# Performance work log

Measured on AMD Instinct MI355X. Metric: run time of the kernel, lower is better.

## Reference

```python
import jax, jax.numpy as jnp
import numpy as np


def _compute_features(ff):
    # ff: (..., 4) = [rx, ry, rvx, rvy]
    rx, ry, rvx, rvy = ff[..., 0], ff[..., 1], ff[..., 2], ff[..., 3]
    dist_sq = rx * rx + ry * ry
    dist = jnp.sqrt(dist_sq + 1e-06)
    inv_dist = 1.0 / (dist + 0.1)
    dir_x = rx / (dist + 1e-06)
    dir_y = ry / (dist + 1e-06)
    speed_sq = rvx * rvx + rvy * rvy
    rel_speed = jnp.sqrt(speed_sq + 1e-06)
    dot_vp = rvx * rx + rvy * ry
    closing_speed = dot_vp / (dist + 1e-06)
    ttca = jnp.tanh(-dot_vp / (speed_sq + 1e-06))
    return jnp.stack(
        [rx, ry, rvx, rvy, dist, inv_dist, rel_speed, closing_speed,
         dir_x, dir_y, ttca, dot_vp], axis=-1)  # (..., 12)


def setup_inputs() -> dict:
    key = jax.random.key(0)
    k0, k1, k2, k3, k4 = jax.random.split(key, 5)
    B, N, H, HID, IN = 16, 256, 8, 64, 12
    ff = jax.random.normal(k0, (B, N, N, 4), dtype=jnp.float32)
    # nn.Linear default init scale ~ 1/sqrt(fan_in); use small random weights
    W1 = jax.random.normal(k1, (IN, HID), dtype=jnp.float32) / np.sqrt(IN)
    b1 = jax.random.normal(k2, (HID,), dtype=jnp.float32) / np.sqrt(IN)
    W2 = jax.random.normal(k3, (HID, H), dtype=jnp.float32) / np.sqrt(HID)
    b2 = jax.random.normal(k4, (H,), dtype=jnp.float32) / np.sqrt(HID)
    return {"fundamental_features": ff, "W1": W1, "b1": b1, "W2": W2, "b2": b2}


def reference(fundamental_features, W1, b1, W2, b2):
    feats = _compute_features(fundamental_features)          # (B, N, N, 12)
    h = jax.nn.silu(jnp.einsum('bnmf,fh->bnmh', feats, W1) + b1)  # (B, N, N, 64)
    bias = jnp.einsum('bnmh,ho->bnmo', h, W2) + b2            # (B, N, N, H)
    return jnp.transpose(bias, (0, 3, 1, 2))                  # (B, H, N, N)
```

## Files before the change

kernel.cpp:

```cpp
#include <hip/hip_runtime.h>

#define NH 8
#define HID 64
#define NPAIRS (16 * 256 * 256)
#define BLOCK 256
#define GPW 4
#define LSTR 68

typedef __attribute__((ext_vector_type(8))) short bf16x8;
typedef __attribute__((ext_vector_type(4))) float f32x4;
typedef __attribute__((ext_vector_type(16))) float f32x16;

union F8 { bf16x8 v; unsigned u[4]; uint4 q4; };

__device__ __host__ inline unsigned bfpk(float a, float b) {
    unsigned ua = __float_as_uint(a); ua += 0x7fffu + ((ua >> 16) & 1u);
    unsigned ub = __float_as_uint(b); ub += 0x7fffu + ((ub >> 16) & 1u);
    return (ua >> 16) | (ub & 0xffff0000u);
}

__global__ void pack_weights(const float* __restrict__ W1, const float* __restrict__ b1,
                             const float* __restrict__ W2, const float* __restrict__ b2,
                             unsigned char* __restrict__ ws) {
    int l = threadIdx.x;
    int n32 = l & 31, q2 = l >> 5;
    int n16 = l & 15, q4 = l >> 4;
    unsigned* B1 = (unsigned*)ws;
    unsigned* B2 = (unsigned*)(ws + 2048);
    float* b1v = (float*)(ws + 4096);
    float* b2v = (float*)(ws + 4608);
    for (int m = 0; m < 2; ++m) {
        int h = m * 32 + n32;
        for (int j2 = 0; j2 < 4; ++j2) {
            int k0 = q2 * 8 + 2 * j2;
            float v0 = (k0 < 12) ? W1[k0 * HID + h] : 0.f;
            float v1 = (k0 + 1 < 12) ? W1[(k0 + 1) * HID + h] : 0.f;
            B1[(m * 64 + l) * 4 + j2] = bfpk(v0, v1);
        }
        b1v[m * 64 + l] = b1[h];
    }
    for (int kc = 0; kc < 2; ++kc)
        for (int j2 = 0; j2 < 4; ++j2) {
            int k0 = kc * 32 + q4 * 8 + 2 * j2;
            float v0 = (n16 < NH) ? W2[k0 * NH + n16] : 0.f;
            float v1 = (n16 < NH) ? W2[(k0 + 1) * NH + n16] : 0.f;
            B2[(kc * 64 + l) * 4 + j2] = bfpk(v0, v1);
        }
    b2v[l] = (n16 < NH) ? b2[n16] : 0.f;
}

__global__ __launch_bounds__(BLOCK) void relfeat_mfma2(
    const float* __restrict__ ff, const unsigned char* __restrict__ ws,
    float* __restrict__ out)
{
    __shared__ float lds[4][32 * LSTR];
    const int tid = threadIdx.x;
    const int w = tid >> 6, l = tid & 63;
    const int n32 = l & 31, q2 = l >> 5;
    const int n16 = l & 15, q4 = l >> 4;
    float* my = lds[w];

    F8 B1f[2], B2f[2];
    #pragma unroll
    for (int m = 0; m < 2; ++m)  B1f[m].q4 = ((const uint4*)ws)[m * 64 + l];
    #pragma unroll
    for (int kc = 0; kc < 2; ++kc) B2f[kc].q4 = ((const uint4*)(ws + 2048))[kc * 64 + l];
    float b1s[2];
    b1s[0] = ((const float*)(ws + 4096))[l];
    b1s[1] = ((const float*)(ws + 4096))[64 + l];
    const float b2s = ((const float*)(ws + 4608))[l];

    f32x16 cbias[2];
    #pragma unroll
    for (int m = 0; m < 2; ++m)
        #pragma unroll
        for (int r = 0; r < 16; ++r) cbias[m][r] = b1s[m];

    const int wave_base = (blockIdx.x * 4 + w) * (GPW * 32);

    for (int g = 0; g < GPW; ++g) {
        const int pbase = wave_base + g * 32;

        float4 v = ((const float4*)ff)[pbase + n32];
        float rx = v.x, ry = v.y, rvx = v.z, rvy = v.w;
        float dist_sq = rx * rx + ry * ry;
        float dist = sqrtf(dist_sq + 1e-6f);
        float speed_sq = rvx * rvx + rvy * rvy;
        float dot_vp = rvx * rx + rvy * ry;
        float invd = __builtin_amdgcn_rcpf(dist + 1e-6f);
        float inv_dist = __builtin_amdgcn_rcpf(dist + 0.1f);
        float rel_speed = sqrtf(speed_sq + 1e-6f);
        float closing = dot_vp * invd;
        float dir_x = rx * invd, dir_y = ry * invd;
        float z = -dot_vp * __builtin_amdgcn_rcpf(speed_sq + 1e-6f);
        float ez = __expf(2.f * z);
        float ttca = 1.f - 2.f * __builtin_amdgcn_rcpf(ez + 1.f);

        F8 a1;
        a1.u[0] = (q2 == 0) ? bfpk(rx, ry)          : bfpk(dir_x, dir_y);
        a1.u[1] = (q2 == 0) ? bfpk(rvx, rvy)        : bfpk(ttca, dot_vp);
        a1.u[2] = (q2 == 0) ? bfpk(dist, inv_dist)  : 0u;
        a1.u[3] = (q2 == 0) ? bfpk(rel_speed, closing) : 0u;

        #pragma unroll
        for (int m = 0; m < 2; ++m) {
            f32x16 d1 = __builtin_amdgcn_mfma_f32_32x32x16_bf16(a1.v, B1f[m].v, cbias[m], 0, 0, 0);
            #pragma unroll
            for (int r = 0; r < 16; ++r) {
                int prow = (r & 3) + 8 * (r >> 2) + 4 * q2;
                float x = d1[r];
                float s = x * __builtin_amdgcn_rcpf(1.f + __expf(-x));
                my[prow * LSTR + m * 32 + n32] = s;
            }
        }

        #pragma unroll
        for (int hl = 0; hl < 2; ++hl) {
            f32x4 d2 = {b2s, b2s, b2s, b2s};
            #pragma unroll
            for (int kc = 0; kc < 2; ++kc) {
                const float* rp = &my[(hl * 16 + n16) * LSTR + kc * 32 + q4 * 8];
                float4 lo = *(const float4*)rp;
                float4 hi = *(const float4*)(rp + 4);
                F8 a2;
                a2.u[0] = bfpk(lo.x, lo.y); a2.u[1] = bfpk(lo.z, lo.w);
                a2.u[2] = bfpk(hi.x, hi.y); a2.u[3] = bfpk(hi.z, hi.w);
                d2 = __builtin_amdgcn_mfma_f32_16x16x32_bf16(a2.v, B2f[kc].v, d2, 0, 0, 0);
            }
            if (n16 < NH) {
                int p0 = pbase + hl * 16 + q4 * 4;
                int b = p0 >> 16, lo16 = p0 & 65535;
                float4 st; st.x = d2[0]; st.y = d2[1]; st.z = d2[2]; st.w = d2[3];
                *(float4*)(out + (size_t)b * (NH * 65536) + (size_t)n16 * 65536 + lo16) = st;
            }
        }
    }
}

extern "C" void kernel_launch(void* const* d_in, const int* in_sizes, int n_in,
                              void* d_out, int out_size, void* d_ws, size_t ws_size,
                              hipStream_t stream) {
    const float* ff = (const float*)d_in[0];
    const float* W1 = (const float*)d_in[1];
    const float* b1 = (const float*)d_in[2];
    const float* W2 = (const float*)d_in[3];
    const float* b2 = (const float*)d_in[4];
    float* out = (float*)d_out;
    unsigned char* ws = (unsigned char*)d_ws;

    pack_weights<<<1, 64, 0, stream>>>(W1, b1, W2, b2, ws);
    const int grid = NPAIRS / (32 * GPW * 4);
    relfeat_mfma2<<<grid, BLOCK, 0, stream>>>(ff, ws, out);
}
```

Measured before the change: 104.8 us.

## Compute features once per lane, fold b1 into GEMM, store hidden as bf16 in LDS

```diff
diff --git a/kernel.cpp b/kernel.cpp
--- a/kernel.cpp
+++ b/kernel.cpp
@@ -1,11 +1,11 @@
 #include <hip/hip_runtime.h>
+#include <hip/hip_bf16.h>
 
 #define NH 8
 #define HID 64
 #define NPAIRS (16 * 256 * 256)
 #define BLOCK 256
-#define GPW 4
-#define LSTR 68
+#define LROW 72
 
 typedef __attribute__((ext_vector_type(8))) short bf16x8;
 typedef __attribute__((ext_vector_type(4))) float f32x4;
@@ -13,10 +13,11 @@
 
 union F8 { bf16x8 v; unsigned u[4]; uint4 q4; };
 
-__device__ __host__ inline unsigned bfpk(float a, float b) {
-    unsigned ua = __float_as_uint(a); ua += 0x7fffu + ((ua >> 16) & 1u);
-    unsigned ub = __float_as_uint(b); ub += 0x7fffu + ((ub >> 16) & 1u);
-    return (ua >> 16) | (ub & 0xffff0000u);
+__device__ inline unsigned pk2(float a, float b) {
+    __hip_bfloat162 h = __float22bfloat162_rn(make_float2(a, b));
+    unsigned u;
+    __builtin_memcpy(&u, &h, 4);
+    return u;
 }
 
 __global__ void pack_weights(const float* __restrict__ W1, const float* __restrict__ b1,
@@ -27,64 +28,57 @@
     int n16 = l & 15, q4 = l >> 4;
     unsigned* B1 = (unsigned*)ws;
     unsigned* B2 = (unsigned*)(ws + 2048);
-    float* b1v = (float*)(ws + 4096);
-    float* b2v = (float*)(ws + 4608);
+    float* b2v = (float*)(ws + 4096);
     for (int m = 0; m < 2; ++m) {
         int h = m * 32 + n32;
         for (int j2 = 0; j2 < 4; ++j2) {
-            int k0 = q2 * 8 + 2 * j2;
-            float v0 = (k0 < 12) ? W1[k0 * HID + h] : 0.f;
-            float v1 = (k0 + 1 < 12) ? W1[(k0 + 1) * HID + h] : 0.f;
-            B1[(m * 64 + l) * 4 + j2] = bfpk(v0, v1);
+            int k0 = q2 * 8 + 2 * j2, k1 = k0 + 1;
+            float v0 = (k0 < 12) ? W1[k0 * HID + h] : (k0 == 12 ? b1[h] : 0.f);
+            float v1 = (k1 < 12) ? W1[k1 * HID + h] : 0.f;
+            B1[(m * 64 + l) * 4 + j2] = pk2(v0, v1);
         }
-        b1v[m * 64 + l] = b1[h];
     }
     for (int kc = 0; kc < 2; ++kc)
         for (int j2 = 0; j2 < 4; ++j2) {
             int k0 = kc * 32 + q4 * 8 + 2 * j2;
             float v0 = (n16 < NH) ? W2[k0 * NH + n16] : 0.f;
             float v1 = (n16 < NH) ? W2[(k0 + 1) * NH + n16] : 0.f;
-            B2[(kc * 64 + l) * 4 + j2] = bfpk(v0, v1);
+            B2[(kc * 64 + l) * 4 + j2] = pk2(v0, v1);
         }
     b2v[l] = (n16 < NH) ? b2[n16] : 0.f;
 }
 
-__global__ __launch_bounds__(BLOCK) void relfeat_mfma2(
+__global__ __launch_bounds__(BLOCK) void relfeat_mfma3(
     const float* __restrict__ ff, const unsigned char* __restrict__ ws,
     float* __restrict__ out)
 {
-    __shared__ float lds[4][32 * LSTR];
+    __shared__ unsigned short lds[4][32 * LROW];
     const int tid = threadIdx.x;
     const int w = tid >> 6, l = tid & 63;
     const int n32 = l & 31, q2 = l >> 5;
     const int n16 = l & 15, q4 = l >> 4;
-    float* my = lds[w];
+    unsigned short* my = lds[w];
 
     F8 B1f[2], B2f[2];
+    B1f[0].q4 = ((const uint4*)ws)[l];
+    B1f[1].q4 = ((const uint4*)ws)[64 + l];
+    B2f[0].q4 = ((const uint4*)(ws + 2048))[l];
+    B2f[1].q4 = ((const uint4*)(ws + 2048))[64 + l];
+    const float b2s = ((const float*)(ws + 4096))[l];
+
+    f32x16 z16;
     #pragma unroll
-    for (int m = 0; m < 2; ++m)  B1f[m].q4 = ((const uint4*)ws)[m * 64 + l];
+    for (int r = 0; r < 16; ++r) z16[r] = 0.f;
+
+    const int wave_base = (blockIdx.x * 4 + w) * 128;
+
     #pragma unroll
-    for (int kc = 0; kc < 2; ++kc) B2f[kc].q4 = ((const uint4*)(ws + 2048))[kc * 64 + l];
-    float b1s[2];
-    b1s[0] = ((const float*)(ws + 4096))[l];
-    b1s[1] = ((const float*)(ws + 4096))[64 + l];
-    const float b2s = ((const float*)(ws + 4608))[l];
+    for (int it = 0; it < 2; ++it) {
+        const int pbase = wave_base + it * 64;
 
-    f32x16 cbias[2];
-    #pragma unroll
-    for (int m = 0; m < 2; ++m)
-        #pragma unroll
-        for (int r = 0; r < 16; ++r) cbias[m][r] = b1s[m];
-
-    const int wave_base = (blockIdx.x * 4 + w) * (GPW * 32);
-
-    for (int g = 0; g < GPW; ++g) {
-        const int pbase = wave_base + g * 32;
-
-        float4 v = ((const float4*)ff)[pbase + n32];
+        float4 v = ((const float4*)ff)[pbase + l];
         float rx = v.x, ry = v.y, rvx = v.z, rvy = v.w;
-        float dist_sq = rx * rx + ry * ry;
-        float dist = sqrtf(dist_sq + 1e-6f);
+        float dist = sqrtf(rx * rx + ry * ry + 1e-6f);
         float speed_sq = rvx * rvx + rvy * rvy;
         float dot_vp = rvx * rx + rvy * ry;
         float invd = __builtin_amdgcn_rcpf(dist + 1e-6f);
@@ -92,46 +86,63 @@
         float rel_speed = sqrtf(speed_sq + 1e-6f);
         float closing = dot_vp * invd;
         float dir_x = rx * invd, dir_y = ry * invd;
-        float z = -dot_vp * __builtin_amdgcn_rcpf(speed_sq + 1e-6f);
-        float ez = __expf(2.f * z);
+        float zz = -dot_vp * __builtin_amdgcn_rcpf(speed_sq + 1e-6f);
+        float ez = __expf(2.f * zz);
         float ttca = 1.f - 2.f * __builtin_amdgcn_rcpf(ez + 1.f);
 
-        F8 a1;
-        a1.u[0] = (q2 == 0) ? bfpk(rx, ry)          : bfpk(dir_x, dir_y);
-        a1.u[1] = (q2 == 0) ? bfpk(rvx, rvy)        : bfpk(ttca, dot_vp);
-        a1.u[2] = (q2 == 0) ? bfpk(dist, inv_dist)  : 0u;
-        a1.u[3] = (q2 == 0) ? bfpk(rel_speed, closing) : 0u;
+        unsigned c0 = pk2(rx, ry), c1 = pk2(rvx, rvy);
+        unsigned c2 = pk2(dist, inv_dist), c3 = pk2(rel_speed, closing);
+        unsigned c4 = pk2(dir_x, dir_y), c5 = pk2(ttca, dot_vp);
+        unsigned sw0 = (unsigned)__shfl_xor((int)c0, 32);
+        unsigned sw1 = (unsigned)__shfl_xor((int)c1, 32);
+        unsigned sw2 = (unsigned)__shfl_xor((int)c2, 32);
+        unsigned sw3 = (unsigned)__shfl_xor((int)c3, 32);
+        unsigned sw4 = (unsigned)__shfl_xor((int)c4, 32);
+        unsigned sw5 = (unsigned)__shfl_xor((int)c5, 32);
+
+        const bool hi = (q2 != 0);
+        F8 frag[2];
+        frag[0].u[0] = hi ? sw4 : c0;
+        frag[0].u[1] = hi ? sw5 : c1;
+        frag[0].u[2] = hi ? 0x00003f80u : c2;
+        frag[0].u[3] = hi ? 0u : c3;
+        frag[1].u[0] = hi ? c4 : sw0;
+        frag[1].u[1] = hi ? c5 : sw1;
+        frag[1].u[2] = hi ? 0x00003f80u : sw2;
+        frag[1].u[3] = hi ? 0u : sw3;
 
         #pragma unroll
-        for (int m = 0; m < 2; ++m) {
-            f32x16 d1 = __builtin_amdgcn_mfma_f32_32x32x16_bf16(a1.v, B1f[m].v, cbias[m], 0, 0, 0);
+        for (int G = 0; G < 2; ++G) {
+            const int pg = pbase + G * 32;
+
             #pragma unroll
-            for (int r = 0; r < 16; ++r) {
-                int prow = (r & 3) + 8 * (r >> 2) + 4 * q2;
-                float x = d1[r];
-                float s = x * __builtin_amdgcn_rcpf(1.f + __expf(-x));
-                my[prow * LSTR + m * 32 + n32] = s;
+            for (int m = 0; m < 2; ++m) {
+                f32x16 d1 = __builtin_amdgcn_mfma_f32_32x32x16_bf16(frag[G].v, B1f[m].v, z16, 0, 0, 0);
+                #pragma unroll
+                for (int r = 0; r < 16; ++r) {
+                    int prow = (r & 3) + 8 * (r >> 2) + 4 * q2;
+                    float x = d1[r];
+                    float s = x * __builtin_amdgcn_rcpf(1.f + __expf(-x));
+                    my[prow * LROW + m * 32 + n32] = (unsigned short)pk2(s, s);
+                }
             }
-        }
 
-        #pragma unroll
-        for (int hl = 0; hl < 2; ++hl) {
-            f32x4 d2 = {b2s, b2s, b2s, b2s};
             #pragma unroll
-            for (int kc = 0; kc < 2; ++kc) {
-                const float* rp = &my[(hl * 16 + n16) * LSTR + kc * 32 + q4 * 8];
-                float4 lo = *(const float4*)rp;
-                float4 hi = *(const float4*)(rp + 4);
-                F8 a2;
-                a2.u[0] = bfpk(lo.x, lo.y); a2.u[1] = bfpk(lo.z, lo.w);
-                a2.u[2] = bfpk(hi.x, hi.y); a2.u[3] = bfpk(hi.z, hi.w);
-                d2 = __builtin_amdgcn_mfma_f32_16x16x32_bf16(a2.v, B2f[kc].v, d2, 0, 0, 0);
-            }
-            if (n16 < NH) {
-                int p0 = pbase + hl * 16 + q4 * 4;
-                int b = p0 >> 16, lo16 = p0 & 65535;
-                float4 st; st.x = d2[0]; st.y = d2[1]; st.z = d2[2]; st.w = d2[3];
-                *(float4*)(out + (size_t)b * (NH * 65536) + (size_t)n16 * 65536 + lo16) = st;
+            for (int hl = 0; hl < 2; ++hl) {
+                f32x4 d2 = {b2s, b2s, b2s, b2s};
+                #pragma unroll
+                for (int kc = 0; kc < 2; ++kc) {
+                    F8 a2;
+                    a2.q4 = *(const uint4*)((const unsigned char*)my
+                              + (hl * 16 + n16) * (LROW * 2) + kc * 64 + q4 * 16);
+                    d2 = __builtin_amdgcn_mfma_f32_16x16x32_bf16(a2.v, B2f[kc].v, d2, 0, 0, 0);
+                }
+                if (n16 < NH) {
+                    int p0 = pg + hl * 16 + q4 * 4;
+                    int b = p0 >> 16, lo16 = p0 & 65535;
+                    float4 st; st.x = d2[0]; st.y = d2[1]; st.z = d2[2]; st.w = d2[3];
+                    *(float4*)(out + (size_t)b * (NH * 65536) + (size_t)n16 * 65536 + lo16) = st;
+                }
             }
         }
     }
@@ -149,6 +160,6 @@
     unsigned char* ws = (unsigned char*)d_ws;
 
     pack_weights<<<1, 64, 0, stream>>>(W1, b1, W2, b2, ws);
-    const int grid = NPAIRS / (32 * GPW * 4);
-    relfeat_mfma2<<<grid, BLOCK, 0, stream>>>(ff, ws, out);
+    const int grid = NPAIRS / (128 * 4);
+    relfeat_mfma3<<<grid, BLOCK, 0, stream>>>(ff, ws, out);
 }
```

Measured after the change: 101.7 us. -3.0%, faster.
